# Optimization experiments

Hardware: AMD Instinct MI355X
Metric: run time of the kernel (lower is better)

The kernel has to match this reference:

```python
import jax, jax.numpy as jnp
import numpy as np

B, T, D, N, L = 8, 2048, 256, 64, 4
LN_EPS = 1e-5


def setup_inputs() -> dict:
    key = jax.random.key(0)
    ks = jax.random.split(key, 8)
    def rn(k, shape, scale=1.0):
        return jax.random.normal(k, shape, dtype=jnp.float32) * scale
    A_init = jnp.log(0.5 + jnp.arange(N, dtype=jnp.float32))  # (N,)
    inp = {
        "sequences": rn(ks[0], (B, T, D)),
        # per-layer stacked params (leading dim L)
        "Wi": rn(ks[1], (L, D, D), 1.0 / np.sqrt(D)),
        "bi": jnp.zeros((L, D), jnp.float32),
        "A_log": jnp.broadcast_to(A_init, (L, D, N)) + 0.0,
        "Cm": rn(ks[2], (L, D, N), 1.0 / np.sqrt(N)),
        "Dp": jnp.ones((L, D), jnp.float32),
        "log_dt": jax.random.uniform(ks[3], (L, D), jnp.float32) * (np.log(0.1) - np.log(0.001)) + np.log(0.001),
        "Wo": rn(ks[4], (L, D, D), 1.0 / np.sqrt(D)),
        "bo": jnp.zeros((L, D), jnp.float32),
        "ln1_g": jnp.ones((L, D), jnp.float32),
        "ln1_b": jnp.zeros((L, D), jnp.float32),
        "ln2_g": jnp.ones((L, D), jnp.float32),
        "ln2_b": jnp.zeros((L, D), jnp.float32),
        "W1": rn(ks[5], (L, D, 4 * D), 1.0 / np.sqrt(D)),
        "b1": jnp.zeros((L, 4 * D), jnp.float32),
        "W2": rn(ks[6], (L, 4 * D, D), 1.0 / np.sqrt(4 * D)),
        "b2": jnp.zeros((L, D), jnp.float32),
        "lnf_g": jnp.ones((D,), jnp.float32),
        "lnf_b": jnp.zeros((D,), jnp.float32),
    }
    return inp


def _ln(x, g, b):
    m = x.mean(-1, keepdims=True)
    v = x.var(-1, keepdims=True)
    return (x - m) / jnp.sqrt(v + LN_EPS) * g + b


def _s4_kernel(A_log_l, Cm_l, log_dt_l, Tlen):
    dt = jnp.exp(log_dt_l)                       # (D,)
    A = -jnp.exp(A_log_l)                        # (D,N)
    A_bar = jnp.exp(A * dt[:, None])             # (D,N)
    B_bar = (A_bar - 1.0) / (A * np.sqrt(N))     # (D,N)
    CB = Cm_l * B_bar                            # (D,N)
    logAb = jnp.log(jnp.clip(A_bar, 1e-10))
    powers = jnp.arange(Tlen, dtype=jnp.float32)
    # (D,N,T) power tensor contracted over N -> (D,T)
    return jnp.einsum('dn,dnt->dt', CB, jnp.exp(logAb[:, :, None] * powers))


def reference(sequences, Wi, bi, A_log, Cm, Dp, log_dt, Wo, bo,
              ln1_g, ln1_b, ln2_g, ln2_b, W1, b1, W2, b2, lnf_g, lnf_b):
    x = sequences  # dropout is identity in eval mode
    Tlen = x.shape[1]
    nfft = 2 * Tlen
    for l in range(L):
        # --- S4D sub-block (pre-norm) ---
        h = _ln(x, ln1_g[l], ln1_b[l])
        u = (h @ Wi[l] + bi[l]).transpose(0, 2, 1)   # (B,D,T)
        K = _s4_kernel(A_log[l], Cm[l], log_dt[l], Tlen)  # (D,T)
        u_f = jnp.fft.rfft(u, n=nfft, axis=-1)
        K_f = jnp.fft.rfft(K, n=nfft, axis=-1)
        y = jnp.fft.irfft(u_f * K_f[None], n=nfft, axis=-1)[..., :Tlen]
        y = y + Dp[l][None, :, None] * u
        y = y.transpose(0, 2, 1) @ Wo[l] + bo[l]
        x = x + y
        # --- MLP sub-block (pre-norm) ---
        h2 = _ln(x, ln2_g[l], ln2_b[l])
        x = x + (jax.nn.gelu(h2 @ W1[l] + b1[l], approximate=False) @ W2[l] + b2[l])
    return _ln(x, lnf_g, lnf_b)
```

## Files before the change

### kernel.cpp

```cpp
#include <hip/hip_runtime.h>
#include <hip/hip_bf16.h>

#define NB 8
#define TT 2048
#define DD 256
#define NN 64
#define LL 4
#define CC 32
#define GG 64
#define BT (NB*TT)

typedef __attribute__((ext_vector_type(8))) short short8;
typedef __attribute__((ext_vector_type(4))) short short4v;
typedef __attribute__((ext_vector_type(4))) float f32x4;

__device__ __forceinline__ float bf2f(__hip_bfloat16 v){ return __bfloat162float(v); }
__device__ __forceinline__ __hip_bfloat16 f2bf(float v){ return __float2bfloat16(v); }
__device__ __forceinline__ short f2bfbits(float v){
  __hip_bfloat16 h = __float2bfloat16(v);
  return __builtin_bit_cast(short, h);
}
__device__ __forceinline__ float bfbits2f(short s){
  __hip_bfloat16 h = __builtin_bit_cast(__hip_bfloat16, s);
  return __bfloat162float(h);
}

#define VMCNT(N) do{ asm volatile("s_waitcnt vmcnt(" #N ")" ::: "memory"); \
                     __builtin_amdgcn_sched_barrier(0); }while(0)
__device__ __forceinline__ void barrier_pre(){
  asm volatile("" ::: "memory");
  __builtin_amdgcn_s_barrier();
  asm volatile("" ::: "memory");
  __builtin_amdgcn_sched_barrier(0);
}
__device__ __forceinline__ void barrier_post(){
  asm volatile("s_waitcnt lgkmcnt(0)" ::: "memory");
  __builtin_amdgcn_sched_barrier(0);
  __builtin_amdgcn_s_barrier();
  asm volatile("" ::: "memory");
  __builtin_amdgcn_sched_barrier(0);
}

__device__ __forceinline__ int get_bf(const void* dtp){
  unsigned u = *(const unsigned*)dtp;
  return ((u >> 16) == (u & 0xFFFFu)) ? 1 : 0;
}

__device__ __forceinline__ float ldin(const void* p, size_t i, int bf){
  return bf ? __bfloat162float(((const __hip_bfloat16*)p)[i]) : ((const float*)p)[i];
}

__device__ __forceinline__ float gelu_f(float x){
  float y = 0.79788456f * fmaf(0.044715f, x*x*x, x);
  float e = __expf(-2.0f * fabsf(y));
  float t = (1.0f - e) / (1.0f + e);
  t = (y >= 0.0f) ? t : -t;
  return 0.5f * x * (1.0f + t);
}

__device__ __forceinline__ void async16(const void* g, void* l){
  __builtin_amdgcn_global_load_lds(
      (const __attribute__((address_space(1))) void*)(unsigned long long)g,
      (__attribute__((address_space(3))) void*)(unsigned long long)l,
      16, 0, 0);
}

__global__ __launch_bounds__(256) void cast_ln_kernel(const void* __restrict__ seq,
    __hip_bfloat16* __restrict__ x, __hip_bfloat16* __restrict__ hN,
    const void* __restrict__ g, const void* __restrict__ b,
    const void* __restrict__ dtp)
{
  int bf = get_bf(dtp);
  int lane = threadIdx.x & 63, w = threadIdx.x >> 6;
  int row = blockIdx.x * 4 + w;
  int c = lane * 4;
  size_t base = (size_t)row*DD + c;
  float v0 = ldin(seq, base+0, bf), v1 = ldin(seq, base+1, bf);
  float v2 = ldin(seq, base+2, bf), v3 = ldin(seq, base+3, bf);
  short4v xk; xk.x=f2bfbits(v0); xk.y=f2bfbits(v1); xk.z=f2bfbits(v2); xk.w=f2bfbits(v3);
  *(short4v*)(x + base) = xk;
  float s = v0+v1+v2+v3;
  #pragma unroll
  for (int o = 1; o < 64; o <<= 1) s += __shfl_xor(s, o);
  float mean = s * (1.0f/DD);
  float d0=v0-mean, d1=v1-mean, d2=v2-mean, d3=v3-mean;
  float sq = d0*d0+d1*d1+d2*d2+d3*d3;
  #pragma unroll
  for (int o = 1; o < 64; o <<= 1) sq += __shfl_xor(sq, o);
  float r = rsqrtf(sq * (1.0f/DD) + 1e-5f);
  short4v hk;
  hk.x = f2bfbits(d0*r*ldin(g,c+0,bf) + ldin(b,c+0,bf));
  hk.y = f2bfbits(d1*r*ldin(g,c+1,bf) + ldin(b,c+1,bf));
  hk.z = f2bfbits(d2*r*ldin(g,c+2,bf) + ldin(b,c+2,bf));
  hk.w = f2bfbits(d3*r*ldin(g,c+3,bf) + ldin(b,c+3,bf));
  *(short4v*)(hN + base) = hk;
}

__global__ __launch_bounds__(256) void transpose_all_kernel(
    const void* __restrict__ Wi, const void* __restrict__ Wo,
    const void* __restrict__ W1, const void* __restrict__ W2,
    __hip_bfloat16* __restrict__ WiT, __hip_bfloat16* __restrict__ WoT,
    __hip_bfloat16* __restrict__ W1T, __hip_bfloat16* __restrict__ W2T,
    const void* __restrict__ dtp)
{
  int bf = get_bf(dtp);
  __shared__ float tile[32][33];
  int id = blockIdx.x;
  const void* W; __hip_bfloat16* Wt; int K, N, l, n0, k0;
  if (id < 256){
    W=Wi; Wt=WiT; K=DD; N=DD;
    int t=id;       l=t>>6; int r=t&63;  n0=(r&7)*32;  k0=(r>>3)*32;
  } else if (id < 512){
    W=Wo; Wt=WoT; K=DD; N=DD;
    int t=id-256;   l=t>>6; int r=t&63;  n0=(r&7)*32;  k0=(r>>3)*32;
  } else if (id < 1536){
    W=W1; Wt=W1T; K=DD; N=4*DD;
    int t=id-512;   l=t>>8; int r=t&255; n0=(r&31)*32; k0=(r>>5)*32;
  } else {
    W=W2; Wt=W2T; K=4*DD; N=DD;
    int t=id-1536;  l=t>>8; int r=t&255; n0=(r&7)*32;  k0=(r>>3)*32;
  }
  size_t zoff = (size_t)l * K * N;
  int tx = threadIdx.x, ty = threadIdx.y;
  #pragma unroll
  for (int i = 0; i < 4; i++)
    tile[ty + i*8][tx] = ldin(W, zoff + (size_t)(k0 + ty + i*8)*N + n0 + tx, bf);
  __syncthreads();
  #pragma unroll
  for (int i = 0; i < 4; i++)
    Wt[zoff + (size_t)(n0 + ty + i*8)*K + k0 + tx] = f2bf(tile[tx][ty + i*8]);
}

__global__ __launch_bounds__(256) void gemm_w1_kernel(
    const __hip_bfloat16* __restrict__ A, const __hip_bfloat16* __restrict__ Wt,
    const void* __restrict__ bias, size_t boff,
    __hip_bfloat16* __restrict__ C, int N, int K, const void* __restrict__ dtp)
{
  int bf = get_bf(dtp);
  __shared__ __align__(16) char smem[49152];
  short (*Als)[2][128][32] = (short(*)[2][128][32])smem;
  short (*Bls)[2][64][32]  = (short(*)[2][64][32])(smem + 32768);
  short* Cls = (short*)smem;
  int tid = threadIdx.x;
  int lane = tid & 63, w = tid >> 6;
  int quad = lane >> 4, row16 = lane & 15;
  int wm = (w >> 1) * 64, wn = (w & 1) * 32;
  int bm = blockIdx.x * 128, bn = blockIdx.y * 64;
  const short* Ag = (const short*)A + (size_t)bm * K;
  const short* Bg = (const short*)Wt + (size_t)bn * K;
  int nt = K >> 6;
  {
    #pragma unroll
    for (int p = 0; p < 4; p++){
      int ch = p*256 + tid; int kc = ch>>9, r=(ch>>2)&127, c=(ch&3)*8;
      async16(Ag + (size_t)r*K + kc*32 + c, &Als[0][kc][r][c]);
    }
    #pragma unroll
    for (int p = 0; p < 2; p++){
      int c2 = p*256 + tid; int k2 = c2>>8, r2=(c2>>2)&63, cc=(c2&3)*8;
      async16(Bg + (size_t)r2*K + k2*32 + cc, &Bls[0][k2][r2][cc]);
    }
  }
  f32x4 acc[4][2] = {};
  for (int t = 0; t < nt; t++){
    int cur = t & 1;
    if (t + 1 < nt){
      int nb_ = cur ^ 1, k0 = (t+1) << 6;
      #pragma unroll
      for (int p = 0; p < 4; p++){
        int ch = p*256 + tid; int kc = ch>>9, r=(ch>>2)&127, c=(ch&3)*8;
        async16(Ag + (size_t)r*K + k0 + kc*32 + c, &Als[nb_][kc][r][c]);
      }
      #pragma unroll
      for (int p = 0; p < 2; p++){
        int c2 = p*256 + tid; int k2 = c2>>8, r2=(c2>>2)&63, cc=(c2&3)*8;
        async16(Bg + (size_t)r2*K + k0 + k2*32 + cc, &Bls[nb_][k2][r2][cc]);
      }
      VMCNT(6);
    } else {
      VMCNT(0);
    }
    barrier_pre();
    #pragma unroll
    for (int kc = 0; kc < 2; kc++){
      short8 af[4], bfr[2];
      #pragma unroll
      for (int i = 0; i < 4; i++)
        af[i] = *(const short8*)&Als[cur][kc][wm + i*16 + row16][quad*8];
      #pragma unroll
      for (int j = 0; j < 2; j++)
        bfr[j] = *(const short8*)&Bls[cur][kc][wn + j*16 + row16][quad*8];
      #pragma unroll
      for (int i = 0; i < 4; i++)
        #pragma unroll
        for (int j = 0; j < 2; j++)
          acc[i][j] = __builtin_amdgcn_mfma_f32_16x16x32_bf16(af[i], bfr[j], acc[i][j], 0, 0, 0);
    }
    barrier_post();
  }
  #pragma unroll
  for (int i = 0; i < 4; i++){
    #pragma unroll
    for (int j = 0; j < 2; j++){
      int col = wn + j*16 + row16;
      float bv = ldin(bias, boff + bn + col, bf);
      #pragma unroll
      for (int r = 0; r < 4; r++){
        int row = wm + i*16 + quad*4 + r;
        Cls[row*72 + col] = f2bfbits(gelu_f(acc[i][j][r] + bv));
      }
    }
  }
  __syncthreads();
  #pragma unroll
  for (int p = 0; p < 4; p++){
    int ch = p*256 + tid;
    int row = ch >> 3, c0 = (ch & 7) * 8;
    short8 v = *(const short8*)&Cls[row*72 + c0];
    *(short8*)&C[(size_t)(bm + row)*N + bn + c0] = v;
  }
}

__global__ __launch_bounds__(256) void gemm_wi_lf_kernel(
    const __hip_bfloat16* __restrict__ A, const __hip_bfloat16* __restrict__ Wt,
    const void* __restrict__ bias, size_t boff,
    __hip_bfloat16* __restrict__ uout, __hip_bfloat16* __restrict__ LFS,
    const float* __restrict__ abT, int K, const void* __restrict__ dtp)
{
  int bf = get_bf(dtp);
  __shared__ __align__(16) char smem[73728];
  short (*Als)[2][32][32]  = (short(*)[2][32][32])smem;
  short (*Bls)[2][256][32] = (short(*)[2][256][32])(smem + 8192);
  float* Cls = (float*)smem;
  int tid = threadIdx.x, lane = tid & 63, w = tid >> 6;
  int quad = lane >> 4, row16 = lane & 15;
  int wn = w * 64;
  int bm = blockIdx.x * 32;
  const short* Ag = (const short*)A + (size_t)bm * K;
  const short* Bg = (const short*)Wt;
  int nt = K >> 6;
  {
    int ch = tid; int kc = ch>>7, r=(ch>>2)&31, c=(ch&3)*8;
    async16(Ag + (size_t)r*K + kc*32 + c, &Als[0][kc][r][c]);
    #pragma unroll
    for (int p = 0; p < 8; p++){
      int c2 = p*256 + tid; int k2 = c2>>10, r2=(c2>>2)&255, cc=(c2&3)*8;
      async16(Bg + (size_t)r2*K + k2*32 + cc, &Bls[0][k2][r2][cc]);
    }
  }
  f32x4 acc[2][4] = {};
  for (int t = 0; t < nt; t++){
    int cur = t & 1;
    if (t + 1 < nt){
      int nb_ = cur ^ 1, k0 = (t+1) << 6;
      int ch = tid; int kc = ch>>7, r=(ch>>2)&31, c=(ch&3)*8;
      async16(Ag + (size_t)r*K + k0 + kc*32 + c, &Als[nb_][kc][r][c]);
      #pragma unroll
      for (int p = 0; p < 8; p++){
        int c2 = p*256 + tid; int k2 = c2>>10, r2=(c2>>2)&255, cc=(c2&3)*8;
        async16(Bg + (size_t)r2*K + k0 + k2*32 + cc, &Bls[nb_][k2][r2][cc]);
      }
      VMCNT(9);
    } else {
      VMCNT(0);
    }
    barrier_pre();
    #pragma unroll
    for (int kc = 0; kc < 2; kc++){
      short8 af[2], bfr[4];
      #pragma unroll
      for (int i = 0; i < 2; i++)
        af[i] = *(const short8*)&Als[cur][kc][i*16 + row16][quad*8];
      #pragma unroll
      for (int j = 0; j < 4; j++)
        bfr[j] = *(const short8*)&Bls[cur][kc][wn + j*16 + row16][quad*8];
      #pragma unroll
      for (int i = 0; i < 2; i++)
        #pragma unroll
        for (int j = 0; j < 4; j++)
          acc[i][j] = __builtin_amdgcn_mfma_f32_16x16x32_bf16(af[i], bfr[j], acc[i][j], 0, 0, 0);
    }
    barrier_post();
  }
  #pragma unroll
  for (int i = 0; i < 2; i++)
    #pragma unroll
    for (int j = 0; j < 4; j++){
      int col = wn + j*16 + row16;
      #pragma unroll
      for (int r = 0; r < 4; r++){
        int row = i*16 + quad*4 + r;
        Cls[row*260 + col] = acc[i][j][r];
      }
    }
  __syncthreads();
  {
    int row = tid >> 3, l7 = tid & 7;
    size_t rbase = (size_t)(bm + row)*DD;
    #pragma unroll
    for (int q = 0; q < 8; q++){
      int c0 = l7*4 + q*32;
      float4 t = *(const float4*)&Cls[row*260 + c0];
      float v0 = t.x + ldin(bias, boff+c0+0, bf);
      float v1 = t.y + ldin(bias, boff+c0+1, bf);
      float v2 = t.z + ldin(bias, boff+c0+2, bf);
      float v3 = t.w + ldin(bias, boff+c0+3, bf);
      float4 wbk; wbk.x=v0; wbk.y=v1; wbk.z=v2; wbk.w=v3;
      *(float4*)&Cls[row*260 + c0] = wbk;
      short4v pk; pk.x=f2bfbits(v0); pk.y=f2bfbits(v1); pk.z=f2bfbits(v2); pk.w=f2bfbits(v3);
      *(short4v*)&uout[rbase + c0] = pk;
    }
  }
  __syncthreads();
  {
    int d = tid;
    int cix = bm >> 5;
    float ab[NN], accn[NN];
    #pragma unroll
    for (int n = 0; n < NN; n++){ ab[n] = abT[n*DD + d]; accn[n] = 0.0f; }
    #pragma unroll 1
    for (int s = 0; s < CC; s++){
      float uv = Cls[s*260 + d];
      #pragma unroll
      for (int n = 0; n < NN; n++) accn[n] = fmaf(ab[n], accn[n], uv);
    }
    #pragma unroll
    for (int n = 0; n < NN; n++)
      LFS[((size_t)cix*NN + n)*DD + d] = f2bf(accn[n]);
  }
}

__global__ __launch_bounds__(256) void s4_scan_kernel(__hip_bfloat16* __restrict__ LFS,
    const float* __restrict__ AbarCT)
{
  int d = threadIdx.x;
  int n = blockIdx.x & (NN-1), b = blockIdx.x >> 6;
  float a = AbarCT[n*DD + d];
  size_t base = ((size_t)(b*GG)*NN + n)*DD + d;
  const size_t gs = (size_t)NN*DD;
  float lf[GG];
  #pragma unroll
  for (int g = 0; g < GG; g++) lf[g] = bf2f(LFS[base + (size_t)g*gs]);
  float s = 0.0f;
  #pragma unroll
  for (int g = 0; g < GG; g++){
    LFS[base + (size_t)g*gs] = f2bf(s);
    s = fmaf(a, s, lf[g]);
  }
}

__global__ __launch_bounds__(512, 4) void gemm_wo_recur_kernel(
    const __hip_bfloat16* __restrict__ uB, const __hip_bfloat16* __restrict__ Sin,
    const float* __restrict__ abT, const float* __restrict__ cbT,
    const void* __restrict__ Dp, size_t dpoff,
    const __hip_bfloat16* __restrict__ Wt, const void* __restrict__ bias, size_t boff,
    const __hip_bfloat16* __restrict__ resx, __hip_bfloat16* __restrict__ xout,
    const void* __restrict__ g, size_t goff, const void* __restrict__ bb, size_t bboff,
    __hip_bfloat16* __restrict__ hout)
{
  int bf = get_bf(Dp);
  __shared__ __align__(16) char smem[50176];
  short* Uls   = (short*)smem;
  short* Afull = (short*)(smem + 16384);
  short* Bext  = (short*)(smem + 32768);
  float* Cls   = (float*)(smem + 16384);
  int tid = threadIdx.x, lane = tid & 63, w = tid >> 6;
  int quad = lane >> 4, row16 = lane & 15;
  int bm = blockIdx.x * CC;
  const short* Bg = (const short*)Wt;
  {
    const short* ug = (const short*)uB + (size_t)bm * DD;
    async16(ug + tid*8,        Uls + tid*8);
    async16(ug + 4096 + tid*8, Uls + 4096 + tid*8);
    #pragma unroll
    for (int p = 0; p < 2; p++){
      int ch = p*512 + tid; int r = ch >> 2, c = (ch & 3) * 8;
      async16(Bg + (size_t)r*DD + c, Bext + ch*8);
    }
  }
  int d = tid >> 1, ng = tid & 1, nb = ng * 32;
  float st[32], ab[32], cb[32];
  {
    const __hip_bfloat16* sbase = Sin + ((size_t)(bm >> 5) * NN + nb)*DD + d;
    const float* abase = abT + (size_t)nb*DD + d;
    const float* cbase = cbT + (size_t)nb*DD + d;
    #pragma unroll
    for (int i = 0; i < 32; i++){
      st[i] = bf2f(sbase[(size_t)i*DD]);
      ab[i] = abase[(size_t)i*DD];
      cb[i] = cbase[(size_t)i*DD];
    }
  }
  float dp = ldin(Dp, dpoff + d, bf);
  __syncthreads();
  {
    short* ya = Afull + (d >> 5)*1024 + (d & 31);
    float uv = bfbits2f(Uls[d]);
    #pragma unroll 1
    for (int tau = 0; tau < CC; tau++){
      float uvn = (tau < CC-1) ? bfbits2f(Uls[(tau+1)*DD + d]) : 0.0f;
      float a0 = 0.0f, a1 = 0.0f, a2 = 0.0f, a3 = 0.0f;
      #pragma unroll
      for (int i = 0; i < 32; i += 4){
        st[i+0] = fmaf(ab[i+0], st[i+0], uv); a0 = fmaf(cb[i+0], st[i+0], a0);
        st[i+1] = fmaf(ab[i+1], st[i+1], uv); a1 = fmaf(cb[i+1], st[i+1], a1);
        st[i+2] = fmaf(ab[i+2], st[i+2], uv); a2 = fmaf(cb[i+2], st[i+2], a2);
        st[i+3] = fmaf(ab[i+3], st[i+3], uv); a3 = fmaf(cb[i+3], st[i+3], a3);
      }
      float tot = (a0 + a1) + (a2 + a3);
      tot += __shfl_xor(tot, 1);
      if (ng == 0) ya[tau*32] = f2bfbits(fmaf(dp, uv, tot));
      uv = uvn;
    }
  }
  __syncthreads();
  int wn = w * 32;
  f32x4 acc[2][2] = {};
  #pragma unroll
  for (int t = 0; t < 8; t++){
    if (t < 7){
      short* nxt = ((t+1) & 1) ? Uls : Bext;
      #pragma unroll
      for (int p = 0; p < 2; p++){
        int ch = p*512 + tid; int r = ch >> 2, c = (ch & 3) * 8;
        async16(Bg + (size_t)r*DD + (t+1)*32 + c, nxt + ch*8);
      }
      VMCNT(2);
    } else {
      VMCNT(0);
    }
    barrier_pre();
    const short* cur = (t & 1) ? Uls : Bext;
    short8 af[2], bfr[2];
    #pragma unroll
    for (int i = 0; i < 2; i++)
      af[i] = *(const short8*)&Afull[t*1024 + (i*16 + row16)*32 + quad*8];
    #pragma unroll
    for (int j = 0; j < 2; j++)
      bfr[j] = *(const short8*)&cur[(wn + j*16 + row16)*32 + quad*8];
    #pragma unroll
    for (int i = 0; i < 2; i++)
      #pragma unroll
      for (int j = 0; j < 2; j++)
        acc[i][j] = __builtin_amdgcn_mfma_f32_16x16x32_bf16(af[i], bfr[j], acc[i][j], 0, 0, 0);
    barrier_post();
  }
  #pragma unroll
  for (int i = 0; i < 2; i++)
    #pragma unroll
    for (int j = 0; j < 2; j++){
      int col = wn + j*16 + row16;
      #pragma unroll
      for (int r = 0; r < 4; r++){
        int row = i*16 + quad*4 + r;
        Cls[row*260 + col] = acc[i][j][r];
      }
    }
  __syncthreads();
  int row = tid >> 4, l4 = tid & 15;
  size_t rbase = (size_t)(bm + row)*DD;
  float v[4][4];
  #pragma unroll
  for (int q = 0; q < 4; q++){
    int c0 = l4*4 + q*64;
    float4 t = *(const float4*)&Cls[row*260 + c0];
    short4v rx = *(const short4v*)&resx[rbase + c0];
    v[q][0] = t.x + ldin(bias, boff+c0+0, bf) + bfbits2f(rx.x);
    v[q][1] = t.y + ldin(bias, boff+c0+1, bf) + bfbits2f(rx.y);
    v[q][2] = t.z + ldin(bias, boff+c0+2, bf) + bfbits2f(rx.z);
    v[q][3] = t.w + ldin(bias, boff+c0+3, bf) + bfbits2f(rx.w);
    short4v pk; pk.x=f2bfbits(v[q][0]); pk.y=f2bfbits(v[q][1]);
    pk.z=f2bfbits(v[q][2]); pk.w=f2bfbits(v[q][3]);
    *(short4v*)&xout[rbase + c0] = pk;
  }
  float s = 0.0f, sq = 0.0f;
  #pragma unroll
  for (int q = 0; q < 4; q++)
    #pragma unroll
    for (int e = 0; e < 4; e++){ s += v[q][e]; sq += v[q][e]*v[q][e]; }
  #pragma unroll
  for (int o = 1; o < 16; o <<= 1){ s += __shfl_xor(s, o); sq += __shfl_xor(sq, o); }
  float mean = s * (1.0f/DD);
  float rstd = rsqrtf(sq * (1.0f/DD) - mean*mean + 1e-5f);
  #pragma unroll
  for (int q = 0; q < 4; q++){
    int c0 = l4*4 + q*64;
    short4v pk;
    pk.x = f2bfbits((v[q][0]-mean)*rstd*ldin(g,goff+c0+0,bf) + ldin(bb,bboff+c0+0,bf));
    pk.y = f2bfbits((v[q][1]-mean)*rstd*ldin(g,goff+c0+1,bf) + ldin(bb,bboff+c0+1,bf));
    pk.z = f2bfbits((v[q][2]-mean)*rstd*ldin(g,goff+c0+2,bf) + ldin(bb,bboff+c0+2,bf));
    pk.w = f2bfbits((v[q][3]-mean)*rstd*ldin(g,goff+c0+3,bf) + ldin(bb,bboff+c0+3,bf));
    *(short4v*)&hout[rbase + c0] = pk;
  }
}

template <int MODE>
__global__ __launch_bounds__(256) void gemm_row_kernel(
    const __hip_bfloat16* __restrict__ A, const __hip_bfloat16* __restrict__ Wt,
    const void* __restrict__ bias, size_t boff,
    const __hip_bfloat16* __restrict__ resx, __hip_bfloat16* __restrict__ xout,
    const void* __restrict__ g, size_t goff,
    const void* __restrict__ bb, size_t bboff,
    __hip_bfloat16* __restrict__ hout, void* __restrict__ vout,
    int K, const void* __restrict__ dtp)
{
  int bf = get_bf(dtp);
  __shared__ __align__(16) char smem[73728];
  short (*Als)[2][32][32]  = (short(*)[2][32][32])smem;
  short (*Bls)[2][256][32] = (short(*)[2][256][32])(smem + 8192);
  float* Cls = (float*)smem;
  int tid = threadIdx.x, lane = tid & 63, w = tid >> 6;
  int quad = lane >> 4, row16 = lane & 15;
  int wn = w * 64;
  int bm = blockIdx.x * 32;
  const short* Ag = (const short*)A + (size_t)bm * K;
  const short* Bg = (const short*)Wt;
  int nt = K >> 6;
  {
    int ch = tid; int kc = ch>>7, r=(ch>>2)&31, c=(ch&3)*8;
    async16(Ag + (size_t)r*K + kc*32 + c, &Als[0][kc][r][c]);
    #pragma unroll
    for (int p = 0; p < 8; p++){
      int c2 = p*256 + tid; int k2 = c2>>10, r2=(c2>>2)&255, cc=(c2&3)*8;
      async16(Bg + (size_t)r2*K + k2*32 + cc, &Bls[0][k2][r2][cc]);
    }
  }
  f32x4 acc[2][4] = {};
  for (int t = 0; t < nt; t++){
    int cur = t & 1;
    if (t + 1 < nt){
      int nb_ = cur ^ 1, k0 = (t+1) << 6;
      int ch = tid; int kc = ch>>7, r=(ch>>2)&31, c=(ch&3)*8;
      async16(Ag + (size_t)r*K + k0 + kc*32 + c, &Als[nb_][kc][r][c]);
      #pragma unroll
      for (int p = 0; p < 8; p++){
        int c2 = p*256 + tid; int k2 = c2>>10, r2=(c2>>2)&255, cc=(c2&3)*8;
        async16(Bg + (size_t)r2*K + k0 + k2*32 + cc, &Bls[nb_][k2][r2][cc]);
      }
      VMCNT(9);
    } else {
      VMCNT(0);
    }
    barrier_pre();
    #pragma unroll
    for (int kc = 0; kc < 2; kc++){
      short8 af[2], bfr[4];
      #pragma unroll
      for (int i = 0; i < 2; i++)
        af[i] = *(const short8*)&Als[cur][kc][i*16 + row16][quad*8];
      #pragma unroll
      for (int j = 0; j < 4; j++)
        bfr[j] = *(const short8*)&Bls[cur][kc][wn + j*16 + row16][quad*8];
      #pragma unroll
      for (int i = 0; i < 2; i++)
        #pragma unroll
        for (int j = 0; j < 4; j++)
          acc[i][j] = __builtin_amdgcn_mfma_f32_16x16x32_bf16(af[i], bfr[j], acc[i][j], 0, 0, 0);
    }
    barrier_post();
  }
  #pragma unroll
  for (int i = 0; i < 2; i++)
    #pragma unroll
    for (int j = 0; j < 4; j++){
      int col = wn + j*16 + row16;
      #pragma unroll
      for (int r = 0; r < 4; r++){
        int row = i*16 + quad*4 + r;
        Cls[row*260 + col] = acc[i][j][r];
      }
    }
  __syncthreads();
  int row = tid >> 3, l7 = tid & 7;
  size_t rbase = (size_t)(bm + row)*DD;
  float v[8][4];
  #pragma unroll
  for (int q = 0; q < 8; q++){
    int c0 = l7*4 + q*32;
    float4 t = *(const float4*)&Cls[row*260 + c0];
    short4v rx = *(const short4v*)&resx[rbase + c0];
    v[q][0] = t.x + ldin(bias, boff+c0+0, bf) + bfbits2f(rx.x);
    v[q][1] = t.y + ldin(bias, boff+c0+1, bf) + bfbits2f(rx.y);
    v[q][2] = t.z + ldin(bias, boff+c0+2, bf) + bfbits2f(rx.z);
    v[q][3] = t.w + ldin(bias, boff+c0+3, bf) + bfbits2f(rx.w);
    if (MODE == 1){
      short4v pk; pk.x=f2bfbits(v[q][0]); pk.y=f2bfbits(v[q][1]);
      pk.z=f2bfbits(v[q][2]); pk.w=f2bfbits(v[q][3]);
      *(short4v*)&xout[rbase + c0] = pk;
    }
  }
  float s = 0.0f, sq = 0.0f;
  #pragma unroll
  for (int q = 0; q < 8; q++)
    #pragma unroll
    for (int e = 0; e < 4; e++){ s += v[q][e]; sq += v[q][e]*v[q][e]; }
  #pragma unroll
  for (int o = 1; o < 8; o <<= 1){ s += __shfl_xor(s, o); sq += __shfl_xor(sq, o); }
  float mean = s * (1.0f/DD);
  float rstd = rsqrtf(sq * (1.0f/DD) - mean*mean + 1e-5f);
  #pragma unroll
  for (int q = 0; q < 8; q++){
    int c0 = l7*4 + q*32;
    float o0 = (v[q][0]-mean)*rstd*ldin(g,goff+c0+0,bf) + ldin(bb,bboff+c0+0,bf);
    float o1 = (v[q][1]-mean)*rstd*ldin(g,goff+c0+1,bf) + ldin(bb,bboff+c0+1,bf);
    float o2 = (v[q][2]-mean)*rstd*ldin(g,goff+c0+2,bf) + ldin(bb,bboff+c0+2,bf);
    float o3 = (v[q][3]-mean)*rstd*ldin(g,goff+c0+3,bf) + ldin(bb,bboff+c0+3,bf);
    if (MODE == 1){
      short4v pk; pk.x=f2bfbits(o0); pk.y=f2bfbits(o1); pk.z=f2bfbits(o2); pk.w=f2bfbits(o3);
      *(short4v*)&hout[rbase + c0] = pk;
    } else {
      if (bf){
        short4v pk; pk.x=f2bfbits(o0); pk.y=f2bfbits(o1); pk.z=f2bfbits(o2); pk.w=f2bfbits(o3);
        *(short4v*)&((__hip_bfloat16*)vout)[rbase + c0] = pk;
      } else {
        float4 pk; pk.x=o0; pk.y=o1; pk.z=o2; pk.w=o3;
        *(float4*)&((float*)vout)[rbase + c0] = pk;
      }
    }
  }
}

__global__ __launch_bounds__(256) void s4_setup_kernel(const void* __restrict__ A_log,
    const void* __restrict__ Cm, const void* __restrict__ log_dt,
    float* __restrict__ AbarT, float* __restrict__ AbarCT, float* __restrict__ cbT,
    const void* __restrict__ dtp)
{
  int bf = get_bf(dtp);
  int d = threadIdx.x, n = blockIdx.x, l = blockIdx.y;
  float dtv = expf(ldin(log_dt, (size_t)l*DD + d, bf));
  float A   = -expf(ldin(A_log, ((size_t)l*DD + d)*NN + n, bf));
  float ab  = expf(A * dtv);
  float bbv = (fabsf(A) > 1e-8f) ? (ab - 1.0f) / (A * 8.0f) : dtv * 0.125f;
  float cb  = ldin(Cm, ((size_t)l*DD + d)*NN + n, bf) * bbv;
  size_t o = ((size_t)l*NN + n)*DD + d;
  AbarT[o] = ab;
  cbT[o]   = cb;
  float p = ab;
  #pragma unroll
  for (int i = 0; i < 5; i++) p *= p;
  AbarCT[o] = p;
}

extern "C" void kernel_launch(void* const* d_in, const int* in_sizes, int n_in,
                              void* d_out, int out_size, void* d_ws, size_t ws_size,
                              hipStream_t stream) {
  const void* seq   = d_in[0];
  const void* Wi    = d_in[1];
  const void* bi    = d_in[2];
  const void* A_log = d_in[3];
  const void* Cm    = d_in[4];
  const void* Dp    = d_in[5];
  const void* logdt = d_in[6];
  const void* Wo    = d_in[7];
  const void* bo    = d_in[8];
  const void* ln1g  = d_in[9];
  const void* ln1b  = d_in[10];
  const void* ln2g  = d_in[11];
  const void* ln2b  = d_in[12];
  const void* W1    = d_in[13];
  const void* b1    = d_in[14];
  const void* W2    = d_in[15];
  const void* b2    = d_in[16];
  const void* lnfg  = d_in[17];
  const void* lnfb  = d_in[18];

  char* ws = (char*)d_ws;
  size_t off = 0;
  __hip_bfloat16* x   = (__hip_bfloat16*)(ws + off); off += (size_t)BT*DD*2;
  __hip_bfloat16* uB  = (__hip_bfloat16*)(ws + off); off += (size_t)BT*DD*2;
  __hip_bfloat16* hN  = (__hip_bfloat16*)(ws + off); off += (size_t)BT*DD*2;
  __hip_bfloat16* mid = (__hip_bfloat16*)(ws + off); off += (size_t)BT*4*DD*2;
  __hip_bfloat16* LFS = (__hip_bfloat16*)(ws + off); off += (size_t)NB*GG*NN*DD*2;
  __hip_bfloat16* WiT = (__hip_bfloat16*)(ws + off); off += (size_t)LL*DD*DD*2;
  __hip_bfloat16* WoT = (__hip_bfloat16*)(ws + off); off += (size_t)LL*DD*DD*2;
  __hip_bfloat16* W1T = (__hip_bfloat16*)(ws + off); off += (size_t)LL*DD*4*DD*2;
  __hip_bfloat16* W2T = (__hip_bfloat16*)(ws + off); off += (size_t)LL*4*DD*DD*2;
  float* AbarT  = (float*)(ws + off); off += (size_t)LL*NN*DD*4;
  float* AbarCT = (float*)(ws + off); off += (size_t)LL*NN*DD*4;
  float* cbT    = (float*)(ws + off); off += (size_t)LL*NN*DD*4;

  (void)in_sizes; (void)n_in; (void)out_size; (void)ws_size;

  cast_ln_kernel<<<BT/4, 256, 0, stream>>>(seq, x, hN, ln1g, ln1b, Dp);
  transpose_all_kernel<<<2560, dim3(32,8), 0, stream>>>(
      Wi, Wo, W1, W2, WiT, WoT, W1T, W2T, Dp);
  s4_setup_kernel<<<dim3(NN, LL), DD, 0, stream>>>(A_log, Cm, logdt, AbarT, AbarCT, cbT, Dp);

  for (int l = 0; l < LL; l++){
    const size_t oD  = (size_t)l*DD;
    const size_t o4D = (size_t)l*4*DD;
    const float* abT  = AbarT  + (size_t)l*NN*DD;
    const float* abCT = AbarCT + (size_t)l*NN*DD;
    const float* cbTl = cbT    + (size_t)l*NN*DD;

    gemm_wi_lf_kernel<<<BT/32, 256, 0, stream>>>(
        hN, WiT + (size_t)l*DD*DD, bi, oD, uB, LFS, abT, DD, Dp);
    s4_scan_kernel<<<NB*NN, 256, 0, stream>>>(LFS, abCT);
    gemm_wo_recur_kernel<<<BT/32, 512, 0, stream>>>(
        uB, LFS, abT, cbTl, Dp, oD,
        WoT + (size_t)l*DD*DD, bo, oD, x, x,
        ln2g, oD, ln2b, oD, hN);

    gemm_w1_kernel<<<dim3(BT/128, 4*DD/64), 256, 0, stream>>>(
        hN, W1T + (size_t)l*DD*4*DD, b1, o4D, mid, 4*DD, DD, Dp);
    if (l < LL-1){
      gemm_row_kernel<1><<<BT/32, 256, 0, stream>>>(
          mid, W2T + (size_t)l*4*DD*DD, b2, oD, x, x,
          ln1g, (size_t)(l+1)*DD, ln1b, (size_t)(l+1)*DD, hN, nullptr, 4*DD, Dp);
    } else {
      gemm_row_kernel<2><<<BT/32, 256, 0, stream>>>(
          mid, W2T + (size_t)l*4*DD*DD, b2, oD, x, nullptr,
          lnfg, 0, lnfb, 0, nullptr, d_out, 4*DD, Dp);
    }
  }
}
```

Baseline: 576.2 us.

## Process two time chunks per block in Wo recurrence GEMM kernel

```diff
diff --git a/kernel.cpp b/kernel.cpp
--- a/kernel.cpp
+++ b/kernel.cpp
@@ -349,7 +349,7 @@
   }
 }
 
-__global__ __launch_bounds__(512, 4) void gemm_wo_recur_kernel(
+__global__ __launch_bounds__(512, 2) void gemm_wo_recur_kernel(
     const __hip_bfloat16* __restrict__ uB, const __hip_bfloat16* __restrict__ Sin,
     const float* __restrict__ abT, const float* __restrict__ cbT,
     const void* __restrict__ Dp, size_t dpoff,
@@ -359,19 +359,24 @@
     __hip_bfloat16* __restrict__ hout)
 {
   int bf = get_bf(Dp);
-  __shared__ __align__(16) char smem[50176];
-  short* Uls   = (short*)smem;
-  short* Afull = (short*)(smem + 16384);
-  short* Bext  = (short*)(smem + 32768);
-  float* Cls   = (float*)(smem + 16384);
+  __shared__ __align__(16) char smem[81920];
+  short* UlsA   = (short*)smem;
+  short* UlsB   = (short*)(smem + 16384);
+  short* AfullA = (short*)(smem + 32768);
+  short* AfullB = (short*)(smem + 49152);
+  short* Bext   = (short*)(smem + 65536);
+  float* Cls    = (float*)smem;
   int tid = threadIdx.x, lane = tid & 63, w = tid >> 6;
   int quad = lane >> 4, row16 = lane & 15;
-  int bm = blockIdx.x * CC;
+  int bm = blockIdx.x * 64;
   const short* Bg = (const short*)Wt;
   {
-    const short* ug = (const short*)uB + (size_t)bm * DD;
-    async16(ug + tid*8,        Uls + tid*8);
-    async16(ug + 4096 + tid*8, Uls + 4096 + tid*8);
+    const short* ugA = (const short*)uB + (size_t)bm * DD;
+    const short* ugB = (const short*)uB + (size_t)(bm + 32) * DD;
+    async16(ugA + tid*8,        UlsA + tid*8);
+    async16(ugA + 4096 + tid*8, UlsA + 4096 + tid*8);
+    async16(ugB + tid*8,        UlsB + tid*8);
+    async16(ugB + 4096 + tid*8, UlsB + 4096 + tid*8);
     #pragma unroll
     for (int p = 0; p < 2; p++){
       int ch = p*512 + tid; int r = ch >> 2, c = (ch & 3) * 8;
@@ -379,47 +384,63 @@
     }
   }
   int d = tid >> 1, ng = tid & 1, nb = ng * 32;
-  float st[32], ab[32], cb[32];
+  float stA[32], stB[32], ab[32], cb[32];
   {
-    const __hip_bfloat16* sbase = Sin + ((size_t)(bm >> 5) * NN + nb)*DD + d;
+    int cix = bm >> 5;
+    const __hip_bfloat16* sA = Sin + ((size_t)cix * NN + nb)*DD + d;
+    const __hip_bfloat16* sB = Sin + ((size_t)(cix + 1) * NN + nb)*DD + d;
     const float* abase = abT + (size_t)nb*DD + d;
     const float* cbase = cbT + (size_t)nb*DD + d;
     #pragma unroll
     for (int i = 0; i < 32; i++){
-      st[i] = bf2f(sbase[(size_t)i*DD]);
-      ab[i] = abase[(size_t)i*DD];
-      cb[i] = cbase[(size_t)i*DD];
+      stA[i] = bf2f(sA[(size_t)i*DD]);
+      stB[i] = bf2f(sB[(size_t)i*DD]);
+      ab[i]  = abase[(size_t)i*DD];
+      cb[i]  = cbase[(size_t)i*DD];
     }
   }
   float dp = ldin(Dp, dpoff + d, bf);
   __syncthreads();
   {
-    short* ya = Afull + (d >> 5)*1024 + (d & 31);
-    float uv = bfbits2f(Uls[d]);
+    int yoff = (d >> 5)*1024 + (d & 31);
+    short* yaA = AfullA + yoff;
+    short* yaB = AfullB + yoff;
+    float uvA = bfbits2f(UlsA[d]);
+    float uvB = bfbits2f(UlsB[d]);
     #pragma unroll 1
     for (int tau = 0; tau < CC; tau++){
-      float uvn = (tau < CC-1) ? bfbits2f(Uls[(tau+1)*DD + d]) : 0.0f;
-      float a0 = 0.0f, a1 = 0.0f, a2 = 0.0f, a3 = 0.0f;
+      float uvAn = (tau < CC-1) ? bfbits2f(UlsA[(tau+1)*DD + d]) : 0.0f;
+      float uvBn = (tau < CC-1) ? bfbits2f(UlsB[(tau+1)*DD + d]) : 0.0f;
+      float a0=0.f,a1=0.f,a2=0.f,a3=0.f, b0=0.f,b1=0.f,b2=0.f,b3=0.f;
       #pragma unroll
       for (int i = 0; i < 32; i += 4){
-        st[i+0] = fmaf(ab[i+0], st[i+0], uv); a0 = fmaf(cb[i+0], st[i+0], a0);
-        st[i+1] = fmaf(ab[i+1], st[i+1], uv); a1 = fmaf(cb[i+1], st[i+1], a1);
-        st[i+2] = fmaf(ab[i+2], st[i+2], uv); a2 = fmaf(cb[i+2], st[i+2], a2);
-        st[i+3] = fmaf(ab[i+3], st[i+3], uv); a3 = fmaf(cb[i+3], st[i+3], a3);
-      }
-      float tot = (a0 + a1) + (a2 + a3);
-      tot += __shfl_xor(tot, 1);
-      if (ng == 0) ya[tau*32] = f2bfbits(fmaf(dp, uv, tot));
-      uv = uvn;
+        stA[i+0] = fmaf(ab[i+0], stA[i+0], uvA); a0 = fmaf(cb[i+0], stA[i+0], a0);
+        stB[i+0] = fmaf(ab[i+0], stB[i+0], uvB); b0 = fmaf(cb[i+0], stB[i+0], b0);
+        stA[i+1] = fmaf(ab[i+1], stA[i+1], uvA); a1 = fmaf(cb[i+1], stA[i+1], a1);
+        stB[i+1] = fmaf(ab[i+1], stB[i+1], uvB); b1 = fmaf(cb[i+1], stB[i+1], b1);
+        stA[i+2] = fmaf(ab[i+2], stA[i+2], uvA); a2 = fmaf(cb[i+2], stA[i+2], a2);
+        stB[i+2] = fmaf(ab[i+2], stB[i+2], uvB); b2 = fmaf(cb[i+2], stB[i+2], b2);
+        stA[i+3] = fmaf(ab[i+3], stA[i+3], uvA); a3 = fmaf(cb[i+3], stA[i+3], a3);
+        stB[i+3] = fmaf(ab[i+3], stB[i+3], uvB); b3 = fmaf(cb[i+3], stB[i+3], b3);
+      }
+      float totA = (a0 + a1) + (a2 + a3);
+      float totB = (b0 + b1) + (b2 + b3);
+      totA += __shfl_xor(totA, 1);
+      totB += __shfl_xor(totB, 1);
+      if (ng == 0){
+        yaA[tau*32] = f2bfbits(fmaf(dp, uvA, totA));
+        yaB[tau*32] = f2bfbits(fmaf(dp, uvB, totB));
+      }
+      uvA = uvAn; uvB = uvBn;
     }
   }
   __syncthreads();
   int wn = w * 32;
-  f32x4 acc[2][2] = {};
+  f32x4 acc[4][2] = {};
   #pragma unroll
   for (int t = 0; t < 8; t++){
     if (t < 7){
-      short* nxt = ((t+1) & 1) ? Uls : Bext;
+      short* nxt = ((t+1) & 1) ? UlsA : Bext;
       #pragma unroll
       for (int p = 0; p < 2; p++){
         int ch = p*512 + tid; int r = ch >> 2, c = (ch & 3) * 8;
@@ -430,23 +451,25 @@
       VMCNT(0);
     }
     barrier_pre();
-    const short* cur = (t & 1) ? Uls : Bext;
-    short8 af[2], bfr[2];
-    #pragma unroll
-    for (int i = 0; i < 2; i++)
-      af[i] = *(const short8*)&Afull[t*1024 + (i*16 + row16)*32 + quad*8];
+    const short* cur = (t & 1) ? UlsA : Bext;
+    short8 af[4], bfr[2];
+    #pragma unroll
+    for (int i = 0; i < 4; i++){
+      const short* Asrc = (i < 2) ? AfullA : AfullB;
+      af[i] = *(const short8*)&Asrc[t*1024 + ((i & 1)*16 + row16)*32 + quad*8];
+    }
     #pragma unroll
     for (int j = 0; j < 2; j++)
       bfr[j] = *(const short8*)&cur[(wn + j*16 + row16)*32 + quad*8];
     #pragma unroll
-    for (int i = 0; i < 2; i++)
+    for (int i = 0; i < 4; i++)
       #pragma unroll
       for (int j = 0; j < 2; j++)
         acc[i][j] = __builtin_amdgcn_mfma_f32_16x16x32_bf16(af[i], bfr[j], acc[i][j], 0, 0, 0);
     barrier_post();
   }
   #pragma unroll
-  for (int i = 0; i < 2; i++)
+  for (int i = 0; i < 4; i++)
     #pragma unroll
     for (int j = 0; j < 2; j++){
       int col = wn + j*16 + row16;
@@ -457,12 +480,12 @@
       }
     }
   __syncthreads();
-  int row = tid >> 4, l4 = tid & 15;
+  int row = tid >> 3, l7 = tid & 7;
   size_t rbase = (size_t)(bm + row)*DD;
-  float v[4][4];
-  #pragma unroll
-  for (int q = 0; q < 4; q++){
-    int c0 = l4*4 + q*64;
+  float v[8][4];
+  #pragma unroll
+  for (int q = 0; q < 8; q++){
+    int c0 = l7*4 + q*32;
     float4 t = *(const float4*)&Cls[row*260 + c0];
     short4v rx = *(const short4v*)&resx[rbase + c0];
     v[q][0] = t.x + ldin(bias, boff+c0+0, bf) + bfbits2f(rx.x);
@@ -475,16 +498,16 @@
   }
   float s = 0.0f, sq = 0.0f;
   #pragma unroll
-  for (int q = 0; q < 4; q++)
+  for (int q = 0; q < 8; q++)
     #pragma unroll
     for (int e = 0; e < 4; e++){ s += v[q][e]; sq += v[q][e]*v[q][e]; }
   #pragma unroll
-  for (int o = 1; o < 16; o <<= 1){ s += __shfl_xor(s, o); sq += __shfl_xor(sq, o); }
+  for (int o = 1; o < 8; o <<= 1){ s += __shfl_xor(s, o); sq += __shfl_xor(sq, o); }
   float mean = s * (1.0f/DD);
   float rstd = rsqrtf(sq * (1.0f/DD) - mean*mean + 1e-5f);
   #pragma unroll
-  for (int q = 0; q < 4; q++){
-    int c0 = l4*4 + q*64;
+  for (int q = 0; q < 8; q++){
+    int c0 = l7*4 + q*32;
     short4v pk;
     pk.x = f2bfbits((v[q][0]-mean)*rstd*ldin(g,goff+c0+0,bf) + ldin(bb,bboff+c0+0,bf));
     pk.y = f2bfbits((v[q][1]-mean)*rstd*ldin(g,goff+c0+1,bf) + ldin(bb,bboff+c0+1,bf));
@@ -696,7 +719,7 @@
     gemm_wi_lf_kernel<<<BT/32, 256, 0, stream>>>(
         hN, WiT + (size_t)l*DD*DD, bi, oD, uB, LFS, abT, DD, Dp);
     s4_scan_kernel<<<NB*NN, 256, 0, stream>>>(LFS, abCT);
-    gemm_wo_recur_kernel<<<BT/32, 512, 0, stream>>>(
+    gemm_wo_recur_kernel<<<BT/64, 512, 0, stream>>>(
         uB, LFS, abT, cbTl, Dp, oD,
         WoT + (size_t)l*DD*DD, bo, oD, x, x,
         ln2g, oD, ln2b, oD, hN);
```

Measured after the change: 594.5 us. 3.2% more time.
